# Optimization experiments

Hardware: AMD Instinct MI355X
Metric: run time of the kernel (lower is better)

Reference implementation:

```python
import jax, jax.numpy as jnp
import numpy as np

B, S, H, R, F, E, K = 4, 2048, 1024, 256, 4096, 8, 2


def setup_inputs() -> dict:
    key = jax.random.key(0)
    k = jax.random.split(key, 7)
    s = 0.02
    return {
        "x": jax.random.normal(k[0], (B, S, H), dtype=jnp.float32),
        "router_w": jax.random.normal(k[1], (H, E), dtype=jnp.float32) * s,
        "router_b": jnp.zeros((E,), dtype=jnp.float32),
        "w1": jax.random.normal(k[2], (E, H, R), dtype=jnp.float32) * s,  # expert Linear(hidden->rank), no bias
        "w2": jax.random.normal(k[3], (E, R, F), dtype=jnp.float32) * s,  # expert Linear(rank->ffn), no bias
        "lin2_w": jax.random.normal(k[4], (F, H), dtype=jnp.float32) * s,
        "lin2_b": jnp.zeros((H,), dtype=jnp.float32),
    }


def reference(x, router_w, router_b, w1, w2, lin2_w, lin2_b):
    # Router: softmax over experts, top-k selection (mask), weight by softmax prob
    logits = jnp.einsum("bsh,he->bse", x, router_w) + router_b
    routing_weights = jax.nn.softmax(logits, axis=-1)            # [B,S,E]
    _, topk_idx = jax.lax.top_k(routing_weights, K)              # [B,S,K]
    mask = jnp.sum(jax.nn.one_hot(topk_idx, E, dtype=x.dtype), axis=-2)  # [B,S,E] in {0,1}
    mw = routing_weights * mask                                  # mask * weight per expert

    # Dense per-expert low-rank FFN (original computes all experts, masks after).
    # Fold mask*weight into the rank-space activations to avoid a [B,S,E,F] tensor.
    t = jnp.einsum("bsh,ehr->bser", x, w1)                       # [B,S,E,R]
    t = t * mw[..., None]
    mixed = jnp.einsum("bser,erf->bsf", t, w2)                   # [B,S,F]

    h = jax.nn.gelu(mixed, approximate=False)                    # torch nn.GELU is erf-based
    out = jnp.einsum("bsf,fh->bsh", h, lin2_w) + lin2_b
    # dropout is identity in eval mode
    return out
```

## Files before the change

kernel.cpp:

```cpp
#include <hip/hip_runtime.h>
#include <math.h>


using short8  = __attribute__((ext_vector_type(8))) short;
using floatx4 = __attribute__((ext_vector_type(4))) float;
typedef unsigned short bf16_t;

#define TOK   8192
#define HDIM  1024
#define RDIM  256
#define FDIM  4096
#define NEXP  8
#define MAXTILES 96
#define MAXSLOTS 16384
#define IMG   16384

__device__ __forceinline__ bf16_t f2bf(float f) {
  union { float f; unsigned u; } a; a.f = f;
  unsigned u = a.u;
  return (bf16_t)((u + 0x7FFFu + ((u >> 16) & 1u)) >> 16);
}

__device__ __forceinline__ float gelu_erf(float v) {
  return 0.5f * v * (1.0f + erff(v * 0.70710678118654752f));
}

__device__ __forceinline__ void gload16(const void* g, void* l) {
  __builtin_amdgcn_global_load_lds(
      (const __attribute__((address_space(1))) void*)g,
      (__attribute__((address_space(3))) void*)l, 16, 0, 0);
}

__device__ __forceinline__ int swz_off(int r, int kl) {
  return r * 128 + ((((kl >> 3) ^ (r & 15)) << 3) | (kl & 7));
}


__device__ __forceinline__ void pack_tile_body(const float* __restrict__ src,
                                               size_t kStride,
                                               bf16_t* __restrict__ img) {
  __shared__ bf16_t lim[IMG];
  const int tid = threadIdx.x;
  const int rr = tid & 127, half = tid >> 7;
  for (int kl = half; kl < 128; kl += 2)
    lim[swz_off(rr, kl)] = f2bf(src[(size_t)kl * kStride + rr]);
  __syncthreads();
  const int4* s4 = (const int4*)lim;
  int4* d4 = (int4*)img;
#pragma unroll
  for (int i = 0; i < 8; i++) d4[tid + i * 256] = s4[tid + i * 256];
}

__global__ void pack_w1(const float* __restrict__ w1, bf16_t* __restrict__ w1p) {
  const int img = blockIdx.x;
  const int e = img >> 4, nc = (img >> 3) & 1, kb = img & 7;
  pack_tile_body(w1 + (size_t)e * 1024 * 256 + (size_t)kb * 128 * 256 + nc * 128,
                 256, w1p + (size_t)img * IMG);
}
__global__ void pack_w2(const float* __restrict__ w2, bf16_t* __restrict__ w2p) {
  const int img = blockIdx.x;
  const int n = img >> 4, e = (img >> 1) & 7, kb = img & 1;
  pack_tile_body(w2 + (size_t)e * 256 * 4096 + (size_t)kb * 128 * 4096 + n * 128,
                 4096, w2p + (size_t)img * IMG);
}

__global__ void tcvt(const float* __restrict__ in, bf16_t* __restrict__ out,
                     int cols, size_t inSlice, size_t ldo,
                     int outRowStep, int outColStep) {
  __shared__ float tile[64][65];
  const int z  = blockIdx.z;
  const float* src = in + (size_t)z * inSlice;
  const int c0 = blockIdx.x * 64;
  const int r0 = blockIdx.y * 64;
  const int tx = threadIdx.x;
  const int ty = threadIdx.y;
#pragma unroll
  for (int i = 0; i < 64; i += 4)
    tile[ty + i][tx] = src[(size_t)(r0 + ty + i) * cols + (c0 + tx)];
  __syncthreads();
#pragma unroll
  for (int i = 0; i < 64; i += 4) {
    float v = tile[tx][ty + i];
    out[((size_t)(c0 + ty + i) + (size_t)z * outRowStep) * ldo +
        (size_t)z * outColStep + (r0 + tx)] = f2bf(v);
  }
}


__global__ void router_kernel(const float* __restrict__ x,
                              const float* __restrict__ rw,
                              const float* __restrict__ rb,
                              int* __restrict__ gid_tok,
                              float2* __restrict__ tokscale,
                              bf16_t* __restrict__ xb) {
  const int token = blockIdx.x * 4 + (threadIdx.x >> 6);
  const int lane  = threadIdx.x & 63;
  const float* xr = x + (size_t)token * HDIM;
  bf16_t* xbr = xb + (size_t)token * HDIM;

  double acc[NEXP];
#pragma unroll
  for (int e = 0; e < NEXP; e++) acc[e] = 0.0;
  for (int h = lane; h < HDIM; h += 64) {
    const float xf = xr[h];
    xbr[h] = f2bf(xf);
    const double xv = (double)xf;
    const float* wr = rw + (size_t)h * NEXP;
#pragma unroll
    for (int e = 0; e < NEXP; e++) acc[e] += xv * (double)wr[e];
  }
#pragma unroll
  for (int off = 32; off > 0; off >>= 1) {
#pragma unroll
    for (int e = 0; e < NEXP; e++) acc[e] += __shfl_xor(acc[e], off, 64);
  }
  double lg[NEXP];
#pragma unroll
  for (int e = 0; e < NEXP; e++) lg[e] = acc[e] + (double)rb[e];

  double mx = lg[0];
#pragma unroll
  for (int e = 1; e < NEXP; e++) mx = fmax(mx, lg[e]);
  double p[NEXP]; double den = 0.0;
#pragma unroll
  for (int e = 0; e < NEXP; e++) { p[e] = exp(lg[e] - mx); den += p[e]; }

  int i1 = 0;
#pragma unroll
  for (int e = 1; e < NEXP; e++) if (lg[e] > lg[i1]) i1 = e;
  int i2 = (i1 == 0) ? 1 : 0;
#pragma unroll
  for (int e = 0; e < NEXP; e++)
    if (e != i1 && e != i2 && lg[e] > lg[i2]) i2 = e;

  if (lane == 0) {
    const int elo = min(i1, i2), ehi = max(i1, i2);
    gid_tok[token] = elo * 8 + ehi;
    tokscale[token] = make_float2((float)(p[elo] / den), (float)(p[ehi] / den));
  }
}

__global__ void build_tiles(const int* __restrict__ gid_tok,
                            int* __restrict__ ctrl,
                            int* __restrict__ tok_of_slot,
                            float2* __restrict__ scale_of_slot) {
  __shared__ int hist[64], ntl[64];
  const int t = threadIdx.x;
  for (int i = t; i < MAXSLOTS; i += 256) {
    tok_of_slot[i] = -1;
    scale_of_slot[i] = make_float2(0.f, 0.f);
  }
  if (t < 64) hist[t] = 0;
  __syncthreads();
  for (int i = t; i < TOK; i += 256) atomicAdd(&hist[gid_tok[i]], 1);
  __syncthreads();
  if (t < 64) ntl[t] = (hist[t] + 127) >> 7;
  __syncthreads();
  if (t < 64) {
    int slot0 = 0, tile0 = 0;
    for (int g = 0; g < t; g++) { slot0 += ntl[g] << 7; tile0 += ntl[g]; }
    ctrl[64 + t] = 0;
    ctrl[128 + t] = slot0;
    const int nt = ntl[t], c = hist[t];
    for (int i = 0; i < nt; i++) {
      ctrl[256 + (tile0 + i) * 3 + 0] = t;
      ctrl[256 + (tile0 + i) * 3 + 1] = slot0 + i * 128;
      ctrl[256 + (tile0 + i) * 3 + 2] = min(128, c - i * 128);
    }
    if (t == 63) ctrl[192] = tile0 + nt;
  }
}

__global__ void scatter_tokens(const int* __restrict__ gid_tok,
                               const float2* __restrict__ tokscale,
                               int* __restrict__ ctrl,
                               int* __restrict__ tok_of_slot,
                               float2* __restrict__ scale_of_slot) {
  const int t = blockIdx.x * 256 + threadIdx.x;
  const int g = gid_tok[t];
  const int pos = atomicAdd(&ctrl[64 + g], 1);
  const int slot = ctrl[128 + g] + pos;
  tok_of_slot[slot] = t;
  scale_of_slot[slot] = tokscale[t];
}

__global__ __launch_bounds__(256)
void gemm_g1(const bf16_t* __restrict__ xb, const bf16_t* __restrict__ w1p,
             bf16_t* __restrict__ Tp, const int* __restrict__ ctrl,
             const int* __restrict__ tok_of_slot,
             const float2* __restrict__ scale_of_slot) {
  const int b = blockIdx.x;
  const int tile = b >> 3, mh = (b >> 2) & 1, n = b & 3;
  if (tile >= ctrl[192]) return;
  const int nrows = ctrl[256 + tile * 3 + 2];
  if (mh && nrows <= 64) return;
  __shared__ bf16_t As[64 * 128];
  __shared__ bf16_t Bs[128 * 128];
  const int gid   = ctrl[256 + tile * 3];
  const int slot0 = ctrl[256 + tile * 3 + 1];
  const int e = (n < 2) ? (gid >> 3) : (gid & 7);
  const int nc = n & 1;
  const int tid = threadIdx.x, lane = tid & 63, w = tid >> 6;
  const int wm = (w & 1) * 32, wn = (w >> 1) * 64;
  const int l16 = lane & 15, quad = lane >> 4;

  floatx4 acc[2][4];
  const floatx4 zero = {0.f, 0.f, 0.f, 0.f};
#pragma unroll
  for (int i = 0; i < 2; i++)
#pragma unroll
    for (int j = 0; j < 4; j++) acc[i][j] = zero;

  int toks[4];
  int rowAs[4];
#pragma unroll
  for (int i = 0; i < 4; i++) {
    rowAs[i] = w * 16 + i * 4 + (lane >> 4);
    int tk = tok_of_slot[slot0 + mh * 64 + rowAs[i]];
    toks[i] = (tk < 0) ? 0 : tk;
  }
  const bf16_t* bimg = w1p + (size_t)(e * 16 + nc * 8) * IMG;
  bf16_t* lA = As + w * 2048;
  bf16_t* lB = Bs + w * 4096;

  for (int kb = 0; kb < 8; kb++) {
    __syncthreads();
#pragma unroll
    for (int i = 0; i < 4; i++) {
      const int gq = (lane & 15) ^ (rowAs[i] & 15);
      gload16(xb + (size_t)toks[i] * HDIM + kb * 128 + gq * 8, lA + i * 512);
    }
#pragma unroll
    for (int i = 0; i < 8; i++)
      gload16(bimg + (size_t)kb * IMG + w * 4096 + i * 512 + lane * 8, lB + i * 512);
    __syncthreads();
#pragma unroll
    for (int s = 0; s < 4; s++) {
      const int pg = ((s * 4 + quad) ^ l16) << 3;
      short8 af[2], bfr[4];
#pragma unroll
      for (int i = 0; i < 2; i++)
        af[i] = *(const short8*)&As[(wm + i * 16 + l16) * 128 + pg];
#pragma unroll
      for (int i = 0; i < 4; i++)
        bfr[i] = *(const short8*)&Bs[(wn + i * 16 + l16) * 128 + pg];
#pragma unroll
      for (int mi = 0; mi < 2; mi++)
#pragma unroll
        for (int ni = 0; ni < 4; ni++)
          acc[mi][ni] = __builtin_amdgcn_mfma_f32_16x16x32_bf16(
              af[mi], bfr[ni], acc[mi][ni], 0, 0, 0);
    }
  }

  __syncthreads();
#pragma unroll
  for (int mi = 0; mi < 2; mi++) {
#pragma unroll
    for (int r = 0; r < 4; r++) {
      const int rloc = wm + mi * 16 + quad * 4 + r;
      const float2 sc = scale_of_slot[slot0 + mh * 64 + rloc];
      const float s = (n < 2) ? sc.x : sc.y;
#pragma unroll
      for (int ni = 0; ni < 4; ni++) {
        const int c = wn + ni * 16 + l16;
        As[swz_off(rloc, c)] = f2bf(acc[mi][ni][r] * s);
      }
    }
  }
  __syncthreads();
  bf16_t* img = Tp + (size_t)(tile * 4 + n) * IMG + mh * 64 * 128;
  const int4* s4 = (const int4*)As;
  int4* d4 = (int4*)img;
#pragma unroll
  for (int j = 0; j < 4; j++) d4[tid + j * 256] = s4[tid + j * 256];
}

__global__ __launch_bounds__(256)
void gemm_g2(const bf16_t* __restrict__ Tp, const bf16_t* __restrict__ w2p,
             bf16_t* __restrict__ Hb, const int* __restrict__ ctrl,
             const int* __restrict__ tok_of_slot) {
  const int b = blockIdx.x;
  const int tile = b >> 6, mh = (b >> 5) & 1, n = b & 31;
  if (tile >= ctrl[192]) return;
  const int nrows = ctrl[256 + tile * 3 + 2];
  if (mh && nrows <= 64) return;
  __shared__ bf16_t As[64 * 128];
  __shared__ bf16_t Bs[128 * 128];
  const int gid   = ctrl[256 + tile * 3];
  const int slot0 = ctrl[256 + tile * 3 + 1];
  const int elo = gid >> 3, ehi = gid & 7;
  const int tid = threadIdx.x, lane = tid & 63, w = tid >> 6;
  const int wm = (w & 1) * 32, wn = (w >> 1) * 64;
  const int l16 = lane & 15, quad = lane >> 4;

  floatx4 acc[2][4];
  const floatx4 zero = {0.f, 0.f, 0.f, 0.f};
#pragma unroll
  for (int i = 0; i < 2; i++)
#pragma unroll
    for (int j = 0; j < 4; j++) acc[i][j] = zero;

  const bf16_t* aimg = Tp + (size_t)tile * 4 * IMG + mh * 64 * 128;
  bf16_t* lA = As + w * 2048;
  bf16_t* lB = Bs + w * 4096;

#pragma unroll
  for (int t = 0; t < 4; t++) {
    const int e = (t < 2) ? elo : ehi;
    const bf16_t* bimg = w2p + (size_t)(n * 16 + e * 2 + (t & 1)) * IMG;
    __syncthreads();
#pragma unroll
    for (int i = 0; i < 4; i++)
      gload16(aimg + (size_t)t * IMG + w * 2048 + i * 512 + lane * 8, lA + i * 512);
#pragma unroll
    for (int i = 0; i < 8; i++)
      gload16(bimg + w * 4096 + i * 512 + lane * 8, lB + i * 512);
    __syncthreads();
#pragma unroll
    for (int s = 0; s < 4; s++) {
      const int pg = ((s * 4 + quad) ^ l16) << 3;
      short8 af[2], bfr[4];
#pragma unroll
      for (int i = 0; i < 2; i++)
        af[i] = *(const short8*)&As[(wm + i * 16 + l16) * 128 + pg];
#pragma unroll
      for (int i = 0; i < 4; i++)
        bfr[i] = *(const short8*)&Bs[(wn + i * 16 + l16) * 128 + pg];
#pragma unroll
      for (int mi = 0; mi < 2; mi++)
#pragma unroll
        for (int ni = 0; ni < 4; ni++)
          acc[mi][ni] = __builtin_amdgcn_mfma_f32_16x16x32_bf16(
              af[mi], bfr[ni], acc[mi][ni], 0, 0, 0);
    }
  }

  __syncthreads();
#pragma unroll
  for (int mi = 0; mi < 2; mi++) {
#pragma unroll
    for (int r = 0; r < 4; r++) {
      const int rloc = wm + mi * 16 + quad * 4 + r;
#pragma unroll
      for (int ni = 0; ni < 4; ni++) {
        const int c = wn + ni * 16 + l16;
        Bs[rloc * 128 + c] = f2bf(gelu_erf(acc[mi][ni][r]));
      }
    }
  }
  __syncthreads();
  const int4* s4 = (const int4*)Bs;
#pragma unroll
  for (int j = 0; j < 4; j++) {
    const int chunk = tid + j * 256;
    const int row = chunk >> 4, off = chunk & 15;
    const int tok = tok_of_slot[slot0 + mh * 64 + row];
    if (tok >= 0)
      *(int4*)(Hb + (size_t)tok * FDIM + n * 128 + off * 8) = s4[chunk];
  }
}

#define MFMA_BF16(a, b, c) __builtin_amdgcn_mfma_f32_16x16x32_bf16(a, b, c, 0, 0, 0)

__global__ __launch_bounds__(512, 1)
void gemm_g3(const bf16_t* __restrict__ Hb, const bf16_t* __restrict__ ltw,
             float* __restrict__ out, const float* __restrict__ bias) {
  __shared__ bf16_t As[3 * 256 * 64];
  __shared__ bf16_t Bs[3 * 128 * 64];

  const int i = blockIdx.x;
  const int xcd = i & 7, j = i >> 3;
  const int m0 = (xcd * 4 + (j >> 3)) * 256;
  const int n0 = (j & 7) * 128;

  const int tid  = threadIdx.x;
  const int lane = tid & 63;
  const int w    = tid >> 6;
  const int l16  = lane & 15;
  const int quad = (lane >> 4) & 3;
  const int WM   = (w & 3) * 64;
  const int WN   = (w >> 2) * 64;

  const int srow = tid >> 3;
  const int sswz = ((tid & 7) ^ (srow & 7)) << 3;
  const bf16_t* ga[4];
  const bf16_t* gb[2];
#pragma unroll
  for (int c = 0; c < 4; c++)
    ga[c] = Hb + (size_t)(m0 + c * 64 + srow) * FDIM + sswz;
#pragma unroll
  for (int c = 0; c < 2; c++)
    gb[c] = ltw + (size_t)(n0 + c * 64 + srow) * FDIM + sswz;
  const int sd = w * 512;

  int aoff[4], boff[4];
#pragma unroll
  for (int mi = 0; mi < 4; mi++) {
    const int r = WM + mi * 16 + l16;
    aoff[mi] = r * 64 + (((((r >> 2) & 1) << 2) | (quad ^ (r & 3))) << 3);
  }
#pragma unroll
  for (int ni = 0; ni < 4; ni++) {
    const int r = WN + ni * 16 + l16;
    boff[ni] = r * 64 + (((((r >> 2) & 1) << 2) | (quad ^ (r & 3))) << 3);
  }

  floatx4 acc[4][4];
  const floatx4 zero = {0.f, 0.f, 0.f, 0.f};
#pragma unroll
  for (int mi = 0; mi < 4; mi++)
#pragma unroll
    for (int ni = 0; ni < 4; ni++) acc[mi][ni] = zero;

  const bf16_t* Ac = As;              const bf16_t* Bc = Bs;
  const bf16_t* An = As + 16384;      const bf16_t* Bn = Bs + 8192;
  bf16_t*       Ag = As + 32768;      bf16_t*       Bg = Bs + 16384;

#pragma unroll
  for (int c = 0; c < 4; c++) { gload16(ga[c], (bf16_t*)As + c * 4096 + sd); ga[c] += 64; }
#pragma unroll
  for (int c = 0; c < 2; c++) { gload16(gb[c], (bf16_t*)Bs + c * 4096 + sd); gb[c] += 64; }
#pragma unroll
  for (int c = 0; c < 4; c++) { gload16(ga[c], (bf16_t*)As + 16384 + c * 4096 + sd); ga[c] += 64; }
#pragma unroll
  for (int c = 0; c < 2; c++) { gload16(gb[c], (bf16_t*)Bs + 8192 + c * 4096 + sd); gb[c] += 64; }
  asm volatile("s_waitcnt vmcnt(6)" ::: "memory");
  __builtin_amdgcn_s_barrier();

  short8 rA[4], rB[4], sA[4], sB[4];
#pragma unroll
  for (int mi = 0; mi < 4; mi++) rA[mi] = *(const short8*)&Ac[aoff[mi]];
#pragma unroll
  for (int ni = 0; ni < 4; ni++) rB[ni] = *(const short8*)&Bc[boff[ni]];

#pragma unroll 1
  for (int kt = 0; kt < 64; ++kt) {
    if (kt < 62) {
#pragma unroll
      for (int c = 0; c < 4; c++) { gload16(ga[c], Ag + c * 4096 + sd); ga[c] += 64; }
#pragma unroll
      for (int c = 0; c < 2; c++) { gload16(gb[c], Bg + c * 4096 + sd); gb[c] += 64; }
    }
#pragma unroll
    for (int mi = 0; mi < 4; mi++) sA[mi] = *(const short8*)&Ac[aoff[mi] ^ 32];
#pragma unroll
    for (int ni = 0; ni < 4; ni++) sB[ni] = *(const short8*)&Bc[boff[ni] ^ 32];
    __builtin_amdgcn_sched_barrier(0);
    __builtin_amdgcn_s_setprio(1);
#pragma unroll
    for (int mi = 0; mi < 4; mi++)
#pragma unroll
      for (int ni = 0; ni < 4; ni++)
        acc[mi][ni] = MFMA_BF16(rA[mi], rB[ni], acc[mi][ni]);
    __builtin_amdgcn_s_setprio(0);
    asm volatile("s_waitcnt lgkmcnt(0)" ::: "memory");
    __builtin_amdgcn_sched_barrier(0);
    if (kt < 62)       asm volatile("s_waitcnt vmcnt(6)" ::: "memory");
    else if (kt == 62) asm volatile("s_waitcnt vmcnt(0)" ::: "memory");
    if (kt < 63) __builtin_amdgcn_s_barrier();
    __builtin_amdgcn_sched_barrier(0);
    if (kt < 63) {
#pragma unroll
      for (int mi = 0; mi < 4; mi++) rA[mi] = *(const short8*)&An[aoff[mi]];
#pragma unroll
      for (int ni = 0; ni < 4; ni++) rB[ni] = *(const short8*)&Bn[boff[ni]];
    }
    __builtin_amdgcn_sched_barrier(0);
    __builtin_amdgcn_s_setprio(1);
#pragma unroll
    for (int mi = 0; mi < 4; mi++)
#pragma unroll
      for (int ni = 0; ni < 4; ni++)
        acc[mi][ni] = MFMA_BF16(sA[mi], sB[ni], acc[mi][ni]);
    __builtin_amdgcn_s_setprio(0);
    const bf16_t* ta = Ac; Ac = An; An = Ag; Ag = (bf16_t*)ta;
    const bf16_t* tb = Bc; Bc = Bn; Bn = Bg; Bg = (bf16_t*)tb;
  }

#pragma unroll
  for (int mi = 0; mi < 4; mi++) {
#pragma unroll
    for (int ni = 0; ni < 4; ni++) {
      const int row = m0 + WM + mi * 16 + quad * 4;
      const int col = n0 + WN + ni * 16 + l16;
      const float bb = bias[col];
#pragma unroll
      for (int r = 0; r < 4; r++)
        out[(size_t)(row + r) * HDIM + col] = acc[mi][ni][r] + bb;
    }
  }
}


extern "C" void kernel_launch(void* const* d_in, const int* in_sizes, int n_in,
                              void* d_out, int out_size, void* d_ws, size_t ws_size,
                              hipStream_t stream) {
  const float* x   = (const float*)d_in[0];
  const float* rw  = (const float*)d_in[1];
  const float* rb  = (const float*)d_in[2];
  const float* w1  = (const float*)d_in[3];
  const float* w2  = (const float*)d_in[4];
  const float* l2w = (const float*)d_in[5];
  const float* l2b = (const float*)d_in[6];

  char* ws = (char*)d_ws;
  int*    ctrl     = (int*)   (ws + 0);
  int*    gid_tok  = (int*)   (ws + 4096);
  float2* tokscale = (float2*)(ws + 36864);
  int*    tokslot  = (int*)   (ws + 102400);
  float2* slotsc   = (float2*)(ws + 167936);
  bf16_t* xb  = (bf16_t*)(ws + 1048576);
  bf16_t* w1p = (bf16_t*)(ws + 17825792);
  bf16_t* w2p = (bf16_t*)(ws + 22020096);
  bf16_t* ltw = (bf16_t*)(ws + 38797312);
  bf16_t* Tp  = (bf16_t*)(ws + 47185920);
  bf16_t* Hb  = (bf16_t*)(ws + 59768832);

  router_kernel<<<TOK / 4, 256, 0, stream>>>(x, rw, rb, gid_tok, tokscale, xb);
  build_tiles<<<1, 256, 0, stream>>>(gid_tok, ctrl, tokslot, slotsc);
  scatter_tokens<<<TOK / 256, 256, 0, stream>>>(gid_tok, tokscale, ctrl, tokslot, slotsc);

  pack_w1<<<128, 256, 0, stream>>>(w1, w1p);
  pack_w2<<<512, 256, 0, stream>>>(w2, w2p);
  tcvt<<<dim3(HDIM / 64, FDIM / 64, 1), dim3(64, 4), 0, stream>>>(
      l2w, ltw, HDIM, 0, FDIM, 0, 0);

  gemm_g1<<<8 * MAXTILES, 256, 0, stream>>>(xb, w1p, Tp, ctrl, tokslot, slotsc);
  gemm_g2<<<64 * MAXTILES, 256, 0, stream>>>(Tp, w2p, Hb, ctrl, tokslot);
  gemm_g3<<<256, 512, 0, stream>>>(Hb, ltw, (float*)d_out, l2b);
}
```

Baseline: 345.3 us.

## Rewrite G2 as triple-buffered 128x256 tile GEMM with 64-wide K packing

The second grouped GEMM now uses 512-thread blocks that each compute a full 128-row by 256-column tile. It runs a three-stage LDS ring with async global-to-LDS loads, explicit waitcnt and barrier control, and register double-buffered fragment reads interleaved with MFMA. To support this, the w2 packing and the G1 output image layout change to 64-wide K chunks with an XOR swizzle, and the GELU output staging uses a swizzled 256-wide layout. The goal is more data reuse per block and overlap of memory latency with matrix math. In exchange the kernel runs at one block per CU with larger LDS use, and the launch grid is coarser.

```diff
diff --git a/kernel.cpp b/kernel.cpp
--- a/kernel.cpp
+++ b/kernel.cpp
@@ -57,11 +57,22 @@
   pack_tile_body(w1 + (size_t)e * 1024 * 256 + (size_t)kb * 128 * 256 + nc * 128,
                  256, w1p + (size_t)img * IMG);
 }
+
 __global__ void pack_w2(const float* __restrict__ w2, bf16_t* __restrict__ w2p) {
+  __shared__ bf16_t lim[8192];
   const int img = blockIdx.x;
-  const int n = img >> 4, e = (img >> 1) & 7, kb = img & 1;
-  pack_tile_body(w2 + (size_t)e * 256 * 4096 + (size_t)kb * 128 * 4096 + n * 128,
-                 4096, w2p + (size_t)img * IMG);
+  const int nb = img >> 5, e = (img >> 2) & 7, rb = img & 3;
+  const float* src = w2 + (size_t)e * 256 * 4096 + (size_t)rb * 64 * 4096 + nb * 128;
+  const int tid = threadIdx.x;
+  const int row = tid & 127, k0 = tid >> 7;
+  for (int k = k0; k < 64; k += 2)
+    lim[row * 64 + ((((k >> 3) ^ (row & 7)) << 3) | (k & 7))] =
+        f2bf(src[(size_t)k * 4096 + row]);
+  __syncthreads();
+  const int4* s4 = (const int4*)lim;
+  int4* d4 = (int4*)(w2p + (size_t)img * 8192);
+#pragma unroll
+  for (int i = 0; i < 4; i++) d4[tid + i * 256] = s4[tid + i * 256];
 }
 
 __global__ void tcvt(const float* __restrict__ in, bf16_t* __restrict__ out,
@@ -264,104 +275,158 @@
 #pragma unroll
       for (int ni = 0; ni < 4; ni++) {
         const int c = wn + ni * 16 + l16;
-        As[swz_off(rloc, c)] = f2bf(acc[mi][ni][r] * s);
+        As[((c >> 6) << 12) + rloc * 64 +
+           (((((c >> 3) & 7) ^ (rloc & 7)) << 3) | (c & 7))] =
+            f2bf(acc[mi][ni][r] * s);
       }
     }
   }
   __syncthreads();
-  bf16_t* img = Tp + (size_t)(tile * 4 + n) * IMG + mh * 64 * 128;
-  const int4* s4 = (const int4*)As;
-  int4* d4 = (int4*)img;
-#pragma unroll
-  for (int j = 0; j < 4; j++) d4[tid + j * 256] = s4[tid + j * 256];
-}
-
-__global__ __launch_bounds__(256)
+  {
+    const int4* s4 = (const int4*)As;
+    int4* d0 = (int4*)(Tp + (size_t)tile * 65536 + (size_t)(n * 2) * 8192 + mh * 4096);
+    int4* d1 = (int4*)(Tp + (size_t)tile * 65536 + (size_t)(n * 2 + 1) * 8192 + mh * 4096);
+    d0[tid] = s4[tid];
+    d0[tid + 256] = s4[tid + 256];
+    d1[tid] = s4[tid + 512];
+    d1[tid + 256] = s4[tid + 768];
+  }
+}
+
+#define MFMA_BF16(a, b, c) __builtin_amdgcn_mfma_f32_16x16x32_bf16(a, b, c, 0, 0, 0)
+
+__global__ __launch_bounds__(512, 1)
 void gemm_g2(const bf16_t* __restrict__ Tp, const bf16_t* __restrict__ w2p,
              bf16_t* __restrict__ Hb, const int* __restrict__ ctrl,
              const int* __restrict__ tok_of_slot) {
+  __shared__ bf16_t As[3 * 8192];
+  __shared__ bf16_t Bs[3 * 16384];
   const int b = blockIdx.x;
-  const int tile = b >> 6, mh = (b >> 5) & 1, n = b & 31;
+  const int tile = b >> 4, nb = b & 15;
   if (tile >= ctrl[192]) return;
-  const int nrows = ctrl[256 + tile * 3 + 2];
-  if (mh && nrows <= 64) return;
-  __shared__ bf16_t As[64 * 128];
-  __shared__ bf16_t Bs[128 * 128];
   const int gid   = ctrl[256 + tile * 3];
   const int slot0 = ctrl[256 + tile * 3 + 1];
   const int elo = gid >> 3, ehi = gid & 7;
+
   const int tid = threadIdx.x, lane = tid & 63, w = tid >> 6;
-  const int wm = (w & 1) * 32, wn = (w >> 1) * 64;
-  const int l16 = lane & 15, quad = lane >> 4;
-
-  floatx4 acc[2][4];
+  const int l16 = lane & 15, quad = (lane >> 4) & 3;
+  const int WM = (w & 1) * 64, WN = (w >> 1) * 64;
+
+  int aoff[4], boff[4];
+#pragma unroll
+  for (int mi = 0; mi < 4; mi++) {
+    const int r = WM + mi * 16 + l16;
+    aoff[mi] = r * 64 + ((quad ^ (r & 7)) << 3);
+  }
+#pragma unroll
+  for (int ni = 0; ni < 4; ni++) {
+    const int r = WN + ni * 16 + l16;
+    boff[ni] = r * 64 + ((quad ^ (r & 7)) << 3);
+  }
+
+  floatx4 acc[4][4];
   const floatx4 zero = {0.f, 0.f, 0.f, 0.f};
 #pragma unroll
-  for (int i = 0; i < 2; i++)
-#pragma unroll
-    for (int j = 0; j < 4; j++) acc[i][j] = zero;
-
-  const bf16_t* aimg = Tp + (size_t)tile * 4 * IMG + mh * 64 * 128;
-  bf16_t* lA = As + w * 2048;
-  bf16_t* lB = Bs + w * 4096;
-
-#pragma unroll
-  for (int t = 0; t < 4; t++) {
-    const int e = (t < 2) ? elo : ehi;
-    const bf16_t* bimg = w2p + (size_t)(n * 16 + e * 2 + (t & 1)) * IMG;
-    __syncthreads();
-#pragma unroll
-    for (int i = 0; i < 4; i++)
-      gload16(aimg + (size_t)t * IMG + w * 2048 + i * 512 + lane * 8, lA + i * 512);
-#pragma unroll
-    for (int i = 0; i < 8; i++)
-      gload16(bimg + w * 4096 + i * 512 + lane * 8, lB + i * 512);
-    __syncthreads();
-#pragma unroll
-    for (int s = 0; s < 4; s++) {
-      const int pg = ((s * 4 + quad) ^ l16) << 3;
-      short8 af[2], bfr[4];
-#pragma unroll
-      for (int i = 0; i < 2; i++)
-        af[i] = *(const short8*)&As[(wm + i * 16 + l16) * 128 + pg];
-#pragma unroll
-      for (int i = 0; i < 4; i++)
-        bfr[i] = *(const short8*)&Bs[(wn + i * 16 + l16) * 128 + pg];
-#pragma unroll
-      for (int mi = 0; mi < 2; mi++)
-#pragma unroll
-        for (int ni = 0; ni < 4; ni++)
-          acc[mi][ni] = __builtin_amdgcn_mfma_f32_16x16x32_bf16(
-              af[mi], bfr[ni], acc[mi][ni], 0, 0, 0);
-    }
-  }
-
-  __syncthreads();
-#pragma unroll
-  for (int mi = 0; mi < 2; mi++) {
-#pragma unroll
-    for (int r = 0; r < 4; r++) {
-      const int rloc = wm + mi * 16 + quad * 4 + r;
-#pragma unroll
-      for (int ni = 0; ni < 4; ni++) {
-        const int c = wn + ni * 16 + l16;
-        Bs[rloc * 128 + c] = f2bf(gelu_erf(acc[mi][ni][r]));
+  for (int mi = 0; mi < 4; mi++)
+#pragma unroll
+    for (int ni = 0; ni < 4; ni++) acc[mi][ni] = zero;
+
+  const bf16_t* Abase = Tp + (size_t)tile * 65536;
+  const int nb2 = nb * 2;
+
+  const bf16_t* Ac = As;             const bf16_t* Bc = Bs;
+  const bf16_t* An = As + 8192;      const bf16_t* Bn = Bs + 16384;
+  bf16_t*       Ag = As + 16384;     bf16_t*       Bg = Bs + 32768;
+
+  auto stage = [&](int ktS, bf16_t* Ad, bf16_t* Bd) {
+    const int e_  = (ktS < 4) ? elo : ehi;
+    const int rb_ = ktS & 3;
+    const bf16_t* as_ = Abase + (size_t)ktS * 8192;
+    const bf16_t* b0_ = w2p + (size_t)(nb2 * 32 + e_ * 4 + rb_) * 8192;
+    const bf16_t* b1_ = w2p + (size_t)((nb2 + 1) * 32 + e_ * 4 + rb_) * 8192;
+    gload16(as_ + tid * 8,        Ad + tid * 8);
+    gload16(as_ + tid * 8 + 4096, Ad + tid * 8 + 4096);
+    gload16(b0_ + tid * 8,        Bd + tid * 8);
+    gload16(b0_ + tid * 8 + 4096, Bd + tid * 8 + 4096);
+    gload16(b1_ + tid * 8,        Bd + tid * 8 + 8192);
+    gload16(b1_ + tid * 8 + 4096, Bd + tid * 8 + 12288);
+  };
+
+  stage(0, (bf16_t*)As, (bf16_t*)Bs);
+  stage(1, (bf16_t*)As + 8192, (bf16_t*)Bs + 16384);
+  asm volatile("s_waitcnt vmcnt(6)" ::: "memory");
+  __builtin_amdgcn_s_barrier();
+
+  short8 rA[4], rB[4], sA[4], sB[4];
+#pragma unroll
+  for (int mi = 0; mi < 4; mi++) rA[mi] = *(const short8*)&Ac[aoff[mi]];
+#pragma unroll
+  for (int ni = 0; ni < 4; ni++) rB[ni] = *(const short8*)&Bc[boff[ni]];
+
+#pragma unroll 1
+  for (int kt = 0; kt < 8; ++kt) {
+    if (kt < 6) stage(kt + 2, Ag, Bg);
+#pragma unroll
+    for (int mi = 0; mi < 4; mi++) sA[mi] = *(const short8*)&Ac[aoff[mi] ^ 32];
+#pragma unroll
+    for (int ni = 0; ni < 4; ni++) sB[ni] = *(const short8*)&Bc[boff[ni] ^ 32];
+    __builtin_amdgcn_sched_barrier(0);
+    __builtin_amdgcn_s_setprio(1);
+#pragma unroll
+    for (int mi = 0; mi < 4; mi++)
+#pragma unroll
+      for (int ni = 0; ni < 4; ni++)
+        acc[mi][ni] = MFMA_BF16(rA[mi], rB[ni], acc[mi][ni]);
+    __builtin_amdgcn_s_setprio(0);
+    asm volatile("s_waitcnt lgkmcnt(0)" ::: "memory");
+    __builtin_amdgcn_sched_barrier(0);
+    if (kt < 6)       asm volatile("s_waitcnt vmcnt(6)" ::: "memory");
+    else if (kt == 6) asm volatile("s_waitcnt vmcnt(0)" ::: "memory");
+    if (kt < 7) __builtin_amdgcn_s_barrier();
+    __builtin_amdgcn_sched_barrier(0);
+    if (kt < 7) {
+#pragma unroll
+      for (int mi = 0; mi < 4; mi++) rA[mi] = *(const short8*)&An[aoff[mi]];
+#pragma unroll
+      for (int ni = 0; ni < 4; ni++) rB[ni] = *(const short8*)&Bn[boff[ni]];
+    }
+    __builtin_amdgcn_sched_barrier(0);
+    __builtin_amdgcn_s_setprio(1);
+#pragma unroll
+    for (int mi = 0; mi < 4; mi++)
+#pragma unroll
+      for (int ni = 0; ni < 4; ni++)
+        acc[mi][ni] = MFMA_BF16(sA[mi], sB[ni], acc[mi][ni]);
+    __builtin_amdgcn_s_setprio(0);
+    const bf16_t* ta = Ac; Ac = An; An = Ag; Ag = (bf16_t*)ta;
+    const bf16_t* tb = Bc; Bc = Bn; Bn = Bg; Bg = (bf16_t*)tb;
+  }
+
+  __syncthreads();
+#pragma unroll
+  for (int mi = 0; mi < 4; mi++)
+#pragma unroll
+    for (int ni = 0; ni < 4; ni++) {
+#pragma unroll
+      for (int r = 0; r < 4; r++) {
+        const int row = WM + mi * 16 + quad * 4 + r;
+        const int col = WN + ni * 16 + l16;
+        Bs[row * 256 + (col ^ (quad << 4))] = f2bf(gelu_erf(acc[mi][ni][r]));
       }
     }
-  }
   __syncthreads();
   const int4* s4 = (const int4*)Bs;
 #pragma unroll
-  for (int j = 0; j < 4; j++) {
-    const int chunk = tid + j * 256;
-    const int row = chunk >> 4, off = chunk & 15;
-    const int tok = tok_of_slot[slot0 + mh * 64 + row];
-    if (tok >= 0)
-      *(int4*)(Hb + (size_t)tok * FDIM + n * 128 + off * 8) = s4[chunk];
-  }
-}
-
-#define MFMA_BF16(a, b, c) __builtin_amdgcn_mfma_f32_16x16x32_bf16(a, b, c, 0, 0, 0)
+  for (int j = 0; j < 8; j++) {
+    const int chunk = tid + j * 512;
+    const int row = chunk >> 5, off = chunk & 31;
+    const int tok = tok_of_slot[slot0 + row];
+    if (tok >= 0) {
+      const int tb = off ^ (((row >> 2) & 3) << 1);
+      *(int4*)(Hb + (size_t)tok * FDIM + nb * 256 + tb * 8) = s4[chunk];
+    }
+  }
+}
 
 __global__ __launch_bounds__(512, 1)
 void gemm_g3(const bf16_t* __restrict__ Hb, const bf16_t* __restrict__ ltw,
@@ -522,11 +587,11 @@
   scatter_tokens<<<TOK / 256, 256, 0, stream>>>(gid_tok, tokscale, ctrl, tokslot, slotsc);
 
   pack_w1<<<128, 256, 0, stream>>>(w1, w1p);
-  pack_w2<<<512, 256, 0, stream>>>(w2, w2p);
+  pack_w2<<<1024, 256, 0, stream>>>(w2, w2p);
   tcvt<<<dim3(HDIM / 64, FDIM / 64, 1), dim3(64, 4), 0, stream>>>(
       l2w, ltw, HDIM, 0, FDIM, 0, 0);
 
   gemm_g1<<<8 * MAXTILES, 256, 0, stream>>>(xb, w1p, Tp, ctrl, tokslot, slotsc);
-  gemm_g2<<<64 * MAXTILES, 256, 0, stream>>>(Tp, w2p, Hb, ctrl, tokslot);
+  gemm_g2<<<16 * MAXTILES, 512, 0, stream>>>(Tp, w2p, Hb, ctrl, tokslot);
   gemm_g3<<<256, 512, 0, stream>>>(Hb, ltw, (float*)d_out, l2b);
 }
```

Measured after the change: 373.2 us. 1.08x slower.

## Repack T and w2 into 64-wide swizzled k-blocks and swizzle g2 epilogue

Applied to the files above, without the earlier changes.

Changes the packed layout of the g1 output (Tp) and the w2 weight images from 128-column swizzled tiles to 64-wide k-blocks with an XOR swizzle keyed on row&7. The g2 operand reads and the global-to-LDS copies follow the new layout. The g2 GELU epilogue now also writes LDS with a column swizzle before the scattered row stores. The aim is fewer LDS bank conflicts on the MFMA operand reads and the epilogue writes. In exchange, pack_w2 launches twice as many smaller blocks, and producer and consumer must agree on the new layout.

```diff
diff --git a/kernel.cpp b/kernel.cpp
--- a/kernel.cpp
+++ b/kernel.cpp
@@ -57,11 +57,22 @@
   pack_tile_body(w1 + (size_t)e * 1024 * 256 + (size_t)kb * 128 * 256 + nc * 128,
                  256, w1p + (size_t)img * IMG);
 }
+
 __global__ void pack_w2(const float* __restrict__ w2, bf16_t* __restrict__ w2p) {
+  __shared__ bf16_t lim[8192];
   const int img = blockIdx.x;
-  const int n = img >> 4, e = (img >> 1) & 7, kb = img & 1;
-  pack_tile_body(w2 + (size_t)e * 256 * 4096 + (size_t)kb * 128 * 4096 + n * 128,
-                 4096, w2p + (size_t)img * IMG);
+  const int nb = img >> 5, e = (img >> 2) & 7, rb = img & 3;
+  const float* src = w2 + (size_t)e * 256 * 4096 + (size_t)rb * 64 * 4096 + nb * 128;
+  const int tid = threadIdx.x;
+  const int row = tid & 127, k0 = tid >> 7;
+  for (int k = k0; k < 64; k += 2)
+    lim[row * 64 + ((((k >> 3) ^ (row & 7)) << 3) | (k & 7))] =
+        f2bf(src[(size_t)k * 4096 + row]);
+  __syncthreads();
+  const int4* s4 = (const int4*)lim;
+  int4* d4 = (int4*)(w2p + (size_t)img * 8192);
+#pragma unroll
+  for (int i = 0; i < 4; i++) d4[tid + i * 256] = s4[tid + i * 256];
 }
 
 __global__ void tcvt(const float* __restrict__ in, bf16_t* __restrict__ out,
@@ -264,35 +275,44 @@
 #pragma unroll
       for (int ni = 0; ni < 4; ni++) {
         const int c = wn + ni * 16 + l16;
-        As[swz_off(rloc, c)] = f2bf(acc[mi][ni][r] * s);
+        As[((c >> 6) << 12) + rloc * 64 +
+           (((((c >> 3) & 7) ^ (rloc & 7)) << 3) | (c & 7))] =
+            f2bf(acc[mi][ni][r] * s);
       }
     }
   }
   __syncthreads();
-  bf16_t* img = Tp + (size_t)(tile * 4 + n) * IMG + mh * 64 * 128;
-  const int4* s4 = (const int4*)As;
-  int4* d4 = (int4*)img;
-#pragma unroll
-  for (int j = 0; j < 4; j++) d4[tid + j * 256] = s4[tid + j * 256];
-}
+  {
+    const int4* s4 = (const int4*)As;
+    int4* d0 = (int4*)(Tp + (size_t)tile * 65536 + (size_t)(n * 2) * 8192 + mh * 4096);
+    int4* d1 = (int4*)(Tp + (size_t)tile * 65536 + (size_t)(n * 2 + 1) * 8192 + mh * 4096);
+    d0[tid] = s4[tid];
+    d0[tid + 256] = s4[tid + 256];
+    d1[tid] = s4[tid + 512];
+    d1[tid + 256] = s4[tid + 768];
+  }
+}
+
+#define MFMA_BF16(a, b, c) __builtin_amdgcn_mfma_f32_16x16x32_bf16(a, b, c, 0, 0, 0)
 
 __global__ __launch_bounds__(256)
 void gemm_g2(const bf16_t* __restrict__ Tp, const bf16_t* __restrict__ w2p,
              bf16_t* __restrict__ Hb, const int* __restrict__ ctrl,
              const int* __restrict__ tok_of_slot) {
+  __shared__ bf16_t As[8192];
+  __shared__ bf16_t Bs[16384];
   const int b = blockIdx.x;
   const int tile = b >> 6, mh = (b >> 5) & 1, n = b & 31;
   if (tile >= ctrl[192]) return;
   const int nrows = ctrl[256 + tile * 3 + 2];
   if (mh && nrows <= 64) return;
-  __shared__ bf16_t As[64 * 128];
-  __shared__ bf16_t Bs[128 * 128];
   const int gid   = ctrl[256 + tile * 3];
   const int slot0 = ctrl[256 + tile * 3 + 1];
   const int elo = gid >> 3, ehi = gid & 7;
+
   const int tid = threadIdx.x, lane = tid & 63, w = tid >> 6;
+  const int l16 = lane & 15, quad = lane >> 4;
   const int wm = (w & 1) * 32, wn = (w >> 1) * 64;
-  const int l16 = lane & 15, quad = lane >> 4;
 
   floatx4 acc[2][4];
   const floatx4 zero = {0.f, 0.f, 0.f, 0.f};
@@ -301,67 +321,74 @@
 #pragma unroll
     for (int j = 0; j < 4; j++) acc[i][j] = zero;
 
-  const bf16_t* aimg = Tp + (size_t)tile * 4 * IMG + mh * 64 * 128;
-  bf16_t* lA = As + w * 2048;
-  bf16_t* lB = Bs + w * 4096;
+  const bf16_t* Abase = Tp + (size_t)tile * 65536 + mh * 4096;
 
 #pragma unroll
   for (int t = 0; t < 4; t++) {
-    const int e = (t < 2) ? elo : ehi;
-    const bf16_t* bimg = w2p + (size_t)(n * 16 + e * 2 + (t & 1)) * IMG;
+    const int e   = (t < 2) ? elo : ehi;
+    const int rb0 = (t & 1) * 2;
     __syncthreads();
 #pragma unroll
     for (int i = 0; i < 4; i++)
-      gload16(aimg + (size_t)t * IMG + w * 2048 + i * 512 + lane * 8, lA + i * 512);
+      gload16(Abase + (size_t)(t * 2 + (w >> 1)) * 8192 +
+                  (w & 1) * 2048 + i * 512 + lane * 8,
+              As + w * 2048 + i * 512);
 #pragma unroll
     for (int i = 0; i < 8; i++)
-      gload16(bimg + w * 4096 + i * 512 + lane * 8, lB + i * 512);
+      gload16(w2p + (size_t)(n * 32 + e * 4 + rb0 + (w >> 1)) * 8192 +
+                  (w & 1) * 4096 + i * 512 + lane * 8,
+              Bs + w * 4096 + i * 512);
     __syncthreads();
 #pragma unroll
     for (int s = 0; s < 4; s++) {
-      const int pg = ((s * 4 + quad) ^ l16) << 3;
       short8 af[2], bfr[4];
 #pragma unroll
-      for (int i = 0; i < 2; i++)
-        af[i] = *(const short8*)&As[(wm + i * 16 + l16) * 128 + pg];
-#pragma unroll
-      for (int i = 0; i < 4; i++)
-        bfr[i] = *(const short8*)&Bs[(wn + i * 16 + l16) * 128 + pg];
+      for (int mi = 0; mi < 2; mi++) {
+        const int r = wm + mi * 16 + l16;
+        af[mi] = *(const short8*)
+            &As[(s >> 1) * 4096 + r * 64 +
+                ((((s & 1) * 4 + quad) ^ (r & 7)) << 3)];
+      }
+#pragma unroll
+      for (int ni = 0; ni < 4; ni++) {
+        const int r = wn + ni * 16 + l16;
+        bfr[ni] = *(const short8*)
+            &Bs[(s >> 1) * 8192 + r * 64 +
+                ((((s & 1) * 4 + quad) ^ (r & 7)) << 3)];
+      }
 #pragma unroll
       for (int mi = 0; mi < 2; mi++)
 #pragma unroll
         for (int ni = 0; ni < 4; ni++)
-          acc[mi][ni] = __builtin_amdgcn_mfma_f32_16x16x32_bf16(
-              af[mi], bfr[ni], acc[mi][ni], 0, 0, 0);
-    }
-  }
-
-  __syncthreads();
-#pragma unroll
-  for (int mi = 0; mi < 2; mi++) {
-#pragma unroll
-    for (int r = 0; r < 4; r++) {
-      const int rloc = wm + mi * 16 + quad * 4 + r;
-#pragma unroll
-      for (int ni = 0; ni < 4; ni++) {
-        const int c = wn + ni * 16 + l16;
-        Bs[rloc * 128 + c] = f2bf(gelu_erf(acc[mi][ni][r]));
+          acc[mi][ni] = MFMA_BF16(af[mi], bfr[ni], acc[mi][ni]);
+    }
+  }
+
+  __syncthreads();
+#pragma unroll
+  for (int mi = 0; mi < 2; mi++)
+#pragma unroll
+    for (int ni = 0; ni < 4; ni++) {
+#pragma unroll
+      for (int r = 0; r < 4; r++) {
+        const int row = wm + mi * 16 + quad * 4 + r;
+        const int col = wn + ni * 16 + l16;
+        Bs[row * 128 + (col ^ (((row >> 2) & 3) << 4))] =
+            f2bf(gelu_erf(acc[mi][ni][r]));
       }
     }
-  }
   __syncthreads();
   const int4* s4 = (const int4*)Bs;
 #pragma unroll
-  for (int j = 0; j < 4; j++) {
-    const int chunk = tid + j * 256;
+  for (int j4 = 0; j4 < 4; j4++) {
+    const int chunk = tid + j4 * 256;
     const int row = chunk >> 4, off = chunk & 15;
     const int tok = tok_of_slot[slot0 + mh * 64 + row];
     if (tok >= 0)
-      *(int4*)(Hb + (size_t)tok * FDIM + n * 128 + off * 8) = s4[chunk];
-  }
-}
-
-#define MFMA_BF16(a, b, c) __builtin_amdgcn_mfma_f32_16x16x32_bf16(a, b, c, 0, 0, 0)
+      *(int4*)(Hb + (size_t)tok * FDIM + n * 128 + off * 8) =
+          s4[(row << 4) | (off ^ (((row >> 2) & 3) << 1))];
+  }
+}
 
 __global__ __launch_bounds__(512, 1)
 void gemm_g3(const bf16_t* __restrict__ Hb, const bf16_t* __restrict__ ltw,
@@ -522,7 +549,7 @@
   scatter_tokens<<<TOK / 256, 256, 0, stream>>>(gid_tok, tokscale, ctrl, tokslot, slotsc);
 
   pack_w1<<<128, 256, 0, stream>>>(w1, w1p);
-  pack_w2<<<512, 256, 0, stream>>>(w2, w2p);
+  pack_w2<<<1024, 256, 0, stream>>>(w2, w2p);
   tcvt<<<dim3(HDIM / 64, FDIM / 64, 1), dim3(64, 4), 0, stream>>>(
       l2w, ltw, HDIM, 0, FDIM, 0, 0);
 
```

After: 341.5 us. Within noise of the previous version (-1.1%).
